# Optimization experiments

Hardware: AMD Instinct MI355X
Metric: run time of the kernel (lower is better)

Reference implementation:

```python
import jax, jax.numpy as jnp
import numpy as np

# VoxelGrid constants (create_empty not shown in source; fixed to a realistic dense grid)
W, L, H = 64, 64, 64
VOXEL_SIZE = 0.05
ORIGIN = 0.0  # per-axis origin, same for all batches
ROUNDING_OFFSET = 0.5
MIN_POINTS_PER_VOXEL = 10


def setup_inputs() -> dict:
    key = jax.random.key(0)
    k1, k2 = jax.random.split(key)
    B, C, N = 4, 32, 200_000
    extent = W * VOXEL_SIZE  # 3.2
    # uniform coords slightly extending past the grid so a few points are OOB
    point_coordinates = jax.random.uniform(
        k1, (B, 3, N), jnp.float32, minval=-0.02, maxval=extent + 0.02)
    point_attributes = jax.random.normal(k2, (B, C, N), jnp.float32)
    return {"point_coordinates": point_coordinates,
            "point_attributes": point_attributes}


def reference(point_coordinates, point_attributes):
    B, C, N = point_attributes.shape
    V = W * L * H
    bounds = jnp.array([W, L, H], jnp.int32)

    # point -> integer voxel coordinates (origin = 0)
    coords = jnp.floor((point_coordinates - ORIGIN) / VOXEL_SIZE
                       + ROUNDING_OFFSET).astype(jnp.int32)      # [B,3,N]
    in_bounds = jnp.all((coords >= 0) & (coords < bounds[None, :, None]),
                        axis=1)                                   # [B,N]
    flat = coords[:, 0] * (L * H) + coords[:, 1] * H + coords[:, 2]
    # route OOB points to segment V which is dropped by segment ops
    flat = jnp.where(in_bounds, flat, V)                          # [B,N]

    def per_batch(idx, attrs, mask):
        # idx [N] int32, attrs [C,N], mask [N] bool
        counts = jax.ops.segment_sum(mask.astype(jnp.int32), idx,
                                     num_segments=V)              # [V]
        vals = jnp.where(mask[None, :], attrs, -jnp.inf)          # [C,N]
        pooled = jax.ops.segment_max(vals.T, idx, num_segments=V).T  # [C,V]
        pooled = jnp.where(counts[None, :] > 0, pooled, jnp.zeros_like(pooled))
        occ = (counts >= MIN_POINTS_PER_VOXEL).astype(attrs.dtype)   # [V]
        return pooled, occ

    data, occ = jax.vmap(per_batch)(flat, point_attributes, in_bounds)
    voxeldata = data.reshape(B, C, W, L, H)
    voxeloccupancy = occ.reshape(B, 1, W, L, H)
    return voxeldata, voxeloccupancy
```

## Files before the change

kernel.cpp:

```cpp
#include <hip/hip_runtime.h>
#include <math.h>


#define GW 64
#define GL 64
#define GH 64
#define GV (GW * GL * GH)
#define NB 4
#define MIN_PTS 10

__device__ __forceinline__ int bin_coord(float x) {
    float m = __fmul_rn(x, 20.0f);
    float r = __fadd_rn(m, 0.5f);
    return (int)floorf(r);
}

__global__ void zero_kernel(uint4* __restrict__ p, int n4) {
    int i = blockIdx.x * blockDim.x + threadIdx.x;
    if (i < n4) p[i] = make_uint4(0u, 0u, 0u, 0u);
}

__global__ void hist_transpose_kernel(const float* __restrict__ coords,
                                      const float* __restrict__ attrs,
                                      int* __restrict__ counts,
                                      int* __restrict__ vox,
                                      int* __restrict__ rank,
                                      float* __restrict__ attrsT,
                                      size_t strideT,
                                      int b0, int N) {
    __shared__ float lds[4][64 * 33];
    int t = threadIdx.x;
    int w = t >> 6;
    int l = t & 63;
    int n = blockIdx.x * 256 + t;
    int b = b0 + blockIdx.y;

    if (n < N) {
        const float* pc = coords + (size_t)b * 3 * N;
        int ix = bin_coord(pc[n]);
        int iy = bin_coord(pc[n + N]);
        int iz = bin_coord(pc[n + 2 * N]);
        bool ok = (unsigned)ix < (unsigned)GW && (unsigned)iy < (unsigned)GL &&
                  (unsigned)iz < (unsigned)GH;
        int v = ok ? ((ix << 12) | (iy << 6) | iz) : -1;
        vox[(size_t)b * N + n] = v;
        if (ok) rank[(size_t)b * N + n] = atomicAdd(&counts[b * GV + v], 1);

        const float* pa = attrs + (size_t)b * 32 * N + n;
        float* row = &lds[w][l * 33];
#pragma unroll
        for (int c = 0; c < 32; ++c)
            row[c] = pa[(size_t)c * N];
    }
    __syncthreads();

    float* dbase = attrsT + (size_t)blockIdx.y * strideT;
    int wbase = blockIdx.x * 256 + w * 64;
    int j = l & 7;
#pragma unroll
    for (int s = 0; s < 8; ++s) {
        int q = s * 8 + (l >> 3);
        int p = wbase + q;
        if (p < N) {
            const float* src = &lds[w][q * 33 + j * 4];
            float4 val = make_float4(src[0], src[1], src[2], src[3]);
            *(float4*)&dbase[(size_t)p * 32 + j * 4] = val;
        }
    }
}

__global__ void hist_kernel(const float* __restrict__ coords,
                            int* __restrict__ counts,
                            int* __restrict__ vox,
                            int* __restrict__ rank,
                            int N) {
    int n = blockIdx.x * blockDim.x + threadIdx.x;
    int b = blockIdx.y;
    if (n >= N) return;
    const float* pc = coords + (size_t)b * 3 * N;
    int ix = bin_coord(pc[n]);
    int iy = bin_coord(pc[n + N]);
    int iz = bin_coord(pc[n + 2 * N]);
    bool ok = (unsigned)ix < (unsigned)GW && (unsigned)iy < (unsigned)GL &&
              (unsigned)iz < (unsigned)GH;
    int v = ok ? ((ix << 12) | (iy << 6) | iz) : -1;
    vox[(size_t)b * N + n] = v;
    if (ok) rank[(size_t)b * N + n] = atomicAdd(&counts[b * GV + v], 1);
}

__global__ void transpose_kernel(const float* __restrict__ attrs,
                                 float* __restrict__ attrsT,
                                 size_t strideT, int b0, int N) {
    __shared__ float lds[4][64 * 33];
    int t = threadIdx.x;
    int w = t >> 6;
    int l = t & 63;
    int n = blockIdx.x * 256 + t;
    int b = b0 + blockIdx.y;
    if (n < N) {
        const float* pa = attrs + (size_t)b * 32 * N + n;
        float* row = &lds[w][l * 33];
#pragma unroll
        for (int c = 0; c < 32; ++c)
            row[c] = pa[(size_t)c * N];
    }
    __syncthreads();
    float* dbase = attrsT + (size_t)blockIdx.y * strideT;
    int wbase = blockIdx.x * 256 + w * 64;
    int j = l & 7;
#pragma unroll
    for (int s = 0; s < 8; ++s) {
        int q = s * 8 + (l >> 3);
        int p = wbase + q;
        if (p < N) {
            const float* src = &lds[w][q * 33 + j * 4];
            float4 val = make_float4(src[0], src[1], src[2], src[3]);
            *(float4*)&dbase[(size_t)p * 32 + j * 4] = val;
        }
    }
}

__global__ void scan_blocks_kernel(const int* __restrict__ counts,
                                   int* __restrict__ offsets,
                                   int* __restrict__ blocksums) {
    __shared__ int lds[256];
    int t = threadIdx.x;
    int base = blockIdx.x * 1024 + t * 4;
    int4 c = *(const int4*)&counts[base];
    int s0 = c.x, s1 = s0 + c.y, s2 = s1 + c.z, s3 = s2 + c.w;
    lds[t] = s3;
    __syncthreads();
    for (int d = 1; d < 256; d <<= 1) {
        int v = (t >= d) ? lds[t - d] : 0;
        __syncthreads();
        if (t >= d) lds[t] += v;
        __syncthreads();
    }
    int excl = (t > 0) ? lds[t - 1] : 0;
    int4 o;
    o.x = excl; o.y = excl + s0; o.z = excl + s1; o.w = excl + s2;
    *(int4*)&offsets[base] = o;
    if (t == 255) blocksums[blockIdx.x] = lds[255];
}

__global__ void scan_sums_kernel(int* __restrict__ blocksums) {
    __shared__ int lds[256];
    int t = threadIdx.x;
    int4 c = *(const int4*)&blocksums[t * 4];
    int s0 = c.x, s1 = s0 + c.y, s2 = s1 + c.z, s3 = s2 + c.w;
    lds[t] = s3;
    __syncthreads();
    for (int d = 1; d < 256; d <<= 1) {
        int v = (t >= d) ? lds[t - d] : 0;
        __syncthreads();
        if (t >= d) lds[t] += v;
        __syncthreads();
    }
    int excl = (t > 0) ? lds[t - 1] : 0;
    int4 o;
    o.x = excl; o.y = excl + s0; o.z = excl + s1; o.w = excl + s2;
    *(int4*)&blocksums[t * 4] = o;
}

__global__ void scan_add_kernel(int* __restrict__ offsets,
                                const int* __restrict__ blocksums) {
    int i = blockIdx.x * blockDim.x + threadIdx.x;
    int s = blocksums[(i * 4) >> 10];
    int4 o = *(int4*)&offsets[i * 4];
    o.x += s; o.y += s; o.z += s; o.w += s;
    *(int4*)&offsets[i * 4] = o;
}

__global__ void scatter_idx_kernel(const int* __restrict__ vox,
                                   const int* __restrict__ rank,
                                   const int* __restrict__ offsets,
                                   int* __restrict__ sorted_idx,
                                   int N) {
    int n = blockIdx.x * blockDim.x + threadIdx.x;
    int b = blockIdx.y;
    if (n >= N) return;
    int v = vox[(size_t)b * N + n];
    if (v < 0) return;
    sorted_idx[offsets[b * GV + v] + rank[(size_t)b * N + n]] = n;
}

__global__ void segmax4_kernel(const float* __restrict__ attrsT,
                               const int* __restrict__ counts,
                               const int* __restrict__ offsets,
                               const int* __restrict__ sorted_idx,
                               float* __restrict__ vdata,
                               float* __restrict__ occ,
                               size_t strideT,
                               int b0) {
    __shared__ float acc[64 * 33];
    __shared__ int cnt_l[64];
    __shared__ int off_l[64];
    __shared__ int sidx[512];
    int t = threadIdx.x;
    int w = t >> 6;
    int l = t & 63;
    int vo = l >> 3;
    int j = l & 7;
    int b = b0 + blockIdx.y;
    int v0 = blockIdx.x * 64;

    if (t < 64) {
        int bv = b * GV + v0 + t;
        cnt_l[t] = counts[bv];
        off_l[t] = offsets[bv];
    }
    __syncthreads();
    int off0 = off_l[0];
    int npts = off_l[63] + cnt_l[63] - off0;

    int vl0 = w * 16 + vo;
    int vl1 = w * 16 + 8 + vo;
    int ks0 = off_l[vl0] - off0, ke0 = ks0 + cnt_l[vl0];
    int ks1 = off_l[vl1] - off0, ke1 = ks1 + cnt_l[vl1];

    float4 m0 = make_float4(-INFINITY, -INFINITY, -INFINITY, -INFINITY);
    float4 m1 = m0;
    const float* sbase = attrsT + (size_t)blockIdx.y * strideT;
    const int* sgl = sorted_idx + off0;

    for (int base = 0; base < npts; base += 512) {
        __syncthreads();
        int mm = npts - base; if (mm > 512) mm = 512;
        for (int i = t; i < mm; i += 256) sidx[i] = sgl[base + i];
        __syncthreads();
        int hi = base + mm;
        int lo0 = ks0 > base ? ks0 : base, h0 = ke0 < hi ? ke0 : hi;
        for (int k = lo0; k < h0; ++k) {
            int idx = sidx[k - base];
            float4 x = *(const float4*)&sbase[(size_t)idx * 32 + j * 4];
            m0.x = fmaxf(m0.x, x.x); m0.y = fmaxf(m0.y, x.y);
            m0.z = fmaxf(m0.z, x.z); m0.w = fmaxf(m0.w, x.w);
        }
        int lo1 = ks1 > base ? ks1 : base, h1 = ke1 < hi ? ke1 : hi;
        for (int k = lo1; k < h1; ++k) {
            int idx = sidx[k - base];
            float4 x = *(const float4*)&sbase[(size_t)idx * 32 + j * 4];
            m1.x = fmaxf(m1.x, x.x); m1.y = fmaxf(m1.y, x.y);
            m1.z = fmaxf(m1.z, x.z); m1.w = fmaxf(m1.w, x.w);
        }
    }

    int c4 = j * 4;
    bool nz0 = cnt_l[vl0] > 0, nz1 = cnt_l[vl1] > 0;
    acc[vl0 * 33 + c4 + 0] = nz0 ? m0.x : 0.0f;
    acc[vl0 * 33 + c4 + 1] = nz0 ? m0.y : 0.0f;
    acc[vl0 * 33 + c4 + 2] = nz0 ? m0.z : 0.0f;
    acc[vl0 * 33 + c4 + 3] = nz0 ? m0.w : 0.0f;
    acc[vl1 * 33 + c4 + 0] = nz1 ? m1.x : 0.0f;
    acc[vl1 * 33 + c4 + 1] = nz1 ? m1.y : 0.0f;
    acc[vl1 * 33 + c4 + 2] = nz1 ? m1.z : 0.0f;
    acc[vl1 * 33 + c4 + 3] = nz1 ? m1.w : 0.0f;
    __syncthreads();

    int vv = v0 + l;
#pragma unroll
    for (int cc = 0; cc < 8; ++cc) {
        int ch = cc * 4 + w;
        vdata[(((size_t)(b * 32 + ch)) << 18) + vv] = acc[l * 33 + ch];
    }
    if (t < 64)
        occ[b * GV + v0 + t] = (cnt_l[t] >= MIN_PTS) ? 1.0f : 0.0f;
}

__global__ void segmax_kernel(const float* __restrict__ attrs,
                              const int* __restrict__ counts,
                              const int* __restrict__ offsets,
                              const int* __restrict__ sorted_idx,
                              float* __restrict__ vdata,
                              float* __restrict__ occ,
                              int N) {
    int t = blockIdx.x * blockDim.x + threadIdx.x;
    int v = t & (GV - 1);
    int c = (t >> 18) & 31;
    int b = t >> 23;
    int bv = (b << 18) | v;
    int cnt = counts[bv];
    int off = offsets[bv];
    const float* row = attrs + ((size_t)(b * 32 + c)) * N;
    float m = -INFINITY;
    for (int k = 0; k < cnt; ++k) {
        m = fmaxf(m, row[sorted_idx[off + k]]);
    }
    vdata[((size_t)(b * 32 + c) << 18) | v] = (cnt > 0) ? m : 0.0f;
    if (c == 0) occ[bv] = (cnt >= MIN_PTS) ? 1.0f : 0.0f;
}

__device__ __forceinline__ unsigned enc_f32(float f) {
    unsigned u = __float_as_uint(f);
    return (u & 0x80000000u) ? ~u : (u | 0x80000000u);
}
__device__ __forceinline__ float dec_f32(unsigned u) {
    return (u & 0x80000000u) ? __uint_as_float(u & 0x7FFFFFFFu)
                             : __uint_as_float(~u);
}

__global__ void init_kernel(uint4* __restrict__ data4, uint4* __restrict__ cnt4,
                            int nData4, int nCnt4) {
    int i = blockIdx.x * blockDim.x + threadIdx.x;
    uint4 z = make_uint4(0u, 0u, 0u, 0u);
    if (i < nData4) data4[i] = z;
    else if (i < nData4 + nCnt4) cnt4[i - nData4] = z;
}

__global__ void scatter_kernel(const float* __restrict__ coords,
                               const float* __restrict__ attrs,
                               unsigned* __restrict__ bits,
                               int* __restrict__ counts,
                               int N, int C) {
    int n = blockIdx.x * blockDim.x + threadIdx.x;
    int b = blockIdx.y;
    if (n >= N) return;
    const float* pc = coords + (size_t)b * 3 * N;
    int ix = bin_coord(pc[n]);
    int iy = bin_coord(pc[n + N]);
    int iz = bin_coord(pc[n + 2 * N]);
    if ((unsigned)ix >= (unsigned)GW || (unsigned)iy >= (unsigned)GL ||
        (unsigned)iz >= (unsigned)GH)
        return;
    int v = (ix << 12) | (iy << 6) | iz;
    atomicAdd(&counts[b * GV + v], 1);
    const float* pa = attrs + (size_t)b * C * N + n;
    unsigned* pb = bits + (size_t)b * C * GV + v;
    for (int c = 0; c < C; ++c)
        atomicMax(&pb[(size_t)c * GV], enc_f32(pa[(size_t)c * N]));
}

__global__ void finalize_kernel(unsigned* __restrict__ data,
                                const int* __restrict__ counts,
                                float* __restrict__ occ, int C) {
    int i = blockIdx.x * blockDim.x + threadIdx.x;
    int nData4 = NB * C * GV / 4;
    int nOcc4 = NB * GV / 4;
    if (i < nData4) {
        int idx = i << 2;
        int v = idx & (GV - 1);
        int b = idx / (C * GV);
        int4 cv = *(const int4*)&counts[b * GV + v];
        uint4 u = *(const uint4*)&data[idx];
        float4 r;
        r.x = cv.x > 0 ? dec_f32(u.x) : 0.0f;
        r.y = cv.y > 0 ? dec_f32(u.y) : 0.0f;
        r.z = cv.z > 0 ? dec_f32(u.z) : 0.0f;
        r.w = cv.w > 0 ? dec_f32(u.w) : 0.0f;
        *(float4*)&data[idx] = r;
    } else if (i < nData4 + nOcc4) {
        int j = (i - nData4) << 2;
        int4 cv = *(const int4*)&counts[j];
        float4 r;
        r.x = cv.x >= MIN_PTS ? 1.0f : 0.0f;
        r.y = cv.y >= MIN_PTS ? 1.0f : 0.0f;
        r.z = cv.z >= MIN_PTS ? 1.0f : 0.0f;
        r.w = cv.w >= MIN_PTS ? 1.0f : 0.0f;
        *(float4*)&occ[j] = r;
    }
}

extern "C" void kernel_launch(void* const* d_in, const int* in_sizes, int n_in,
                              void* d_out, int out_size, void* d_ws, size_t ws_size,
                              hipStream_t stream) {
    const float* coords = (const float*)d_in[0];
    const float* attrs  = (const float*)d_in[1];
    int N = in_sizes[0] / (NB * 3);
    int C = in_sizes[1] / (NB * N);

    size_t wsCommon = (size_t)(2 * NB * GV + 4096 + 3 * NB * N) * 4;
    size_t oneT  = (size_t)N * 32 * 4;
    size_t fullT = (size_t)NB * N * 32 * 4;

    if (C == 32 && ws_size >= wsCommon + oneT) {
        int* counts     = (int*)d_ws;
        int* offsets    = counts + (size_t)NB * GV;
        int* blocksums  = offsets + (size_t)NB * GV;
        int* vox        = blocksums + 4096;
        int* rank       = vox + (size_t)NB * N;
        int* sorted_idx = rank + (size_t)NB * N;
        float* attrsT   = (float*)(sorted_idx + (size_t)NB * N);
        float* vdata    = (float*)d_out;
        float* occ      = (float*)d_out + (size_t)NB * 32 * GV;

        int nCnt4 = NB * GV / 4;
        zero_kernel<<<(nCnt4 + 255) / 256, 256, 0, stream>>>((uint4*)counts,
                                                             nCnt4);
        dim3 pgrid((N + 255) / 256, NB);
        bool full = (ws_size >= wsCommon + fullT);

        if (full) {
            hist_transpose_kernel<<<pgrid, 256, 0, stream>>>(
                coords, attrs, counts, vox, rank, attrsT, (size_t)N * 32, 0, N);
        } else {
            hist_kernel<<<pgrid, 256, 0, stream>>>(coords, counts, vox, rank,
                                                   N);
        }

        scan_blocks_kernel<<<NB * GV / 1024, 256, 0, stream>>>(counts, offsets,
                                                               blocksums);
        scan_sums_kernel<<<1, 256, 0, stream>>>(blocksums);
        scan_add_kernel<<<NB * GV / 1024, 256, 0, stream>>>(offsets, blocksums);

        scatter_idx_kernel<<<pgrid, 256, 0, stream>>>(vox, rank, offsets,
                                                      sorted_idx, N);

        if (full) {
            segmax4_kernel<<<dim3(GV / 64, NB), 256, 0, stream>>>(
                attrsT, counts, offsets, sorted_idx, vdata, occ,
                (size_t)N * 32, 0);
        } else {
            for (int b = 0; b < NB; ++b) {
                transpose_kernel<<<dim3((N + 255) / 256, 1), 256, 0, stream>>>(
                    attrs, attrsT, 0, b, N);
                segmax4_kernel<<<dim3(GV / 64, 1), 256, 0, stream>>>(
                    attrsT, counts, offsets, sorted_idx, vdata, occ, 0, b);
            }
        }
    } else if (C == 32 &&
               ws_size >= (size_t)(2 * NB * GV + 4096 + 3 * NB * N) * 4) {
        int* counts     = (int*)d_ws;
        int* offsets    = counts + (size_t)NB * GV;
        int* blocksums  = offsets + (size_t)NB * GV;
        int* vox        = blocksums + 4096;
        int* rank       = vox + (size_t)NB * N;
        int* sorted_idx = rank + (size_t)NB * N;
        float* vdata    = (float*)d_out;
        float* occ      = (float*)d_out + (size_t)NB * 32 * GV;

        int nCnt4 = NB * GV / 4;
        zero_kernel<<<(nCnt4 + 255) / 256, 256, 0, stream>>>((uint4*)counts,
                                                             nCnt4);
        dim3 pgrid((N + 255) / 256, NB);
        hist_kernel<<<pgrid, 256, 0, stream>>>(coords, counts, vox, rank, N);

        scan_blocks_kernel<<<NB * GV / 1024, 256, 0, stream>>>(counts, offsets,
                                                               blocksums);
        scan_sums_kernel<<<1, 256, 0, stream>>>(blocksums);
        scan_add_kernel<<<NB * GV / 1024, 256, 0, stream>>>(offsets, blocksums);

        scatter_idx_kernel<<<pgrid, 256, 0, stream>>>(vox, rank, offsets,
                                                      sorted_idx, N);

        int segThreads = NB * 32 * GV;
        segmax_kernel<<<segThreads / 256, 256, 0, stream>>>(
            attrs, counts, offsets, sorted_idx, vdata, occ, N);
    } else {
        unsigned* bits = (unsigned*)d_out;
        float* occ = (float*)d_out + (size_t)NB * C * GV;
        int* counts = (int*)d_ws;
        int nData4 = NB * C * GV / 4;
        int nCnt4 = NB * GV / 4;
        int initTotal = nData4 + nCnt4;
        init_kernel<<<(initTotal + 255) / 256, 256, 0, stream>>>(
            (uint4*)d_out, (uint4*)d_ws, nData4, nCnt4);
        dim3 sgrid((N + 255) / 256, NB);
        scatter_kernel<<<sgrid, 256, 0, stream>>>(coords, attrs, bits, counts,
                                                  N, C);
        finalize_kernel<<<(initTotal + 255) / 256, 256, 0, stream>>>(
            bits, counts, occ, C);
    }
}
```

Measured before the change: 300.5 us.

## Fuse the whole voxel pooling pipeline into one cooperative persistent kernel

Replaces the sequence of zero, histogram/transpose, three-stage scan, index scatter and segment-max launches with a single cooperative kernel. The phases are separated by grid-wide syncs and the blocks loop persistently over the work. This is meant to remove per-launch overhead and inter-kernel gaps. In exchange, the grid is capped at occupancy (max 2048 blocks), which can reduce latency hiding in the memory-bound gather phase, and each grid.sync has its own cost. A fallback to the old multi-kernel path remains if the cooperative launch fails.

```diff
diff --git a/kernel.cpp b/kernel.cpp
--- a/kernel.cpp
+++ b/kernel.cpp
@@ -1,4 +1,5 @@
 #include <hip/hip_runtime.h>
+#include <hip/hip_cooperative_groups.h>
 #include <math.h>
 
 
@@ -9,11 +10,214 @@
 #define NB 4
 #define MIN_PTS 10
 
+namespace cg = cooperative_groups;
+
 __device__ __forceinline__ int bin_coord(float x) {
     float m = __fmul_rn(x, 20.0f);
     float r = __fadd_rn(m, 0.5f);
     return (int)floorf(r);
 }
+
+union MegaSmem {
+    float tr[4][64 * 33];
+    int scan[256];
+    struct {
+        float acc[64 * 33];
+        int cnt[64];
+        int off[64];
+        int sidx[512];
+    } sm;
+};
+
+__global__ void __launch_bounds__(256, 4)
+mega_kernel(const float* __restrict__ coords,
+            const float* __restrict__ attrs,
+            int* __restrict__ counts,
+            int* __restrict__ offsets,
+            int* __restrict__ blocksums,
+            int* __restrict__ vox,
+            int* __restrict__ rank,
+            int* __restrict__ sorted_idx,
+            float* __restrict__ attrsT,
+            float* __restrict__ vdata,
+            float* __restrict__ occ,
+            int N) {
+    cg::grid_group grid = cg::this_grid();
+    __shared__ MegaSmem S;
+    const int t = threadIdx.x;
+    const int G = gridDim.x;
+    const int bid = blockIdx.x;
+    const size_t strideT = (size_t)N * 32;
+
+    {
+        uint4* c4 = (uint4*)counts;
+        for (int i = bid * 256 + t; i < NB * GV / 4; i += G * 256)
+            c4[i] = make_uint4(0u, 0u, 0u, 0u);
+    }
+    grid.sync();
+
+    const int perB = (N + 255) / 256;
+    const int w = t >> 6, l = t & 63;
+    for (int vb = bid; vb < NB * perB; vb += G) {
+        int b = vb / perB;
+        int blk = vb - b * perB;
+        int n = blk * 256 + t;
+        if (n < N) {
+            const float* pc = coords + (size_t)b * 3 * N;
+            int ix = bin_coord(pc[n]);
+            int iy = bin_coord(pc[n + N]);
+            int iz = bin_coord(pc[n + 2 * N]);
+            bool ok = (unsigned)ix < (unsigned)GW &&
+                      (unsigned)iy < (unsigned)GL &&
+                      (unsigned)iz < (unsigned)GH;
+            int v = ok ? ((ix << 12) | (iy << 6) | iz) : -1;
+            vox[(size_t)b * N + n] = v;
+            if (ok) rank[(size_t)b * N + n] = atomicAdd(&counts[b * GV + v], 1);
+            const float* pa = attrs + (size_t)b * 32 * N + n;
+            float* row = &S.tr[w][l * 33];
+#pragma unroll
+            for (int c = 0; c < 32; ++c)
+                row[c] = pa[(size_t)c * N];
+        }
+        __syncthreads();
+        float* dbase = attrsT + (size_t)b * strideT;
+        int wbase = blk * 256 + w * 64;
+        int j = l & 7;
+#pragma unroll
+        for (int s = 0; s < 8; ++s) {
+            int q = s * 8 + (l >> 3);
+            int p = wbase + q;
+            if (p < N) {
+                const float* src = &S.tr[w][q * 33 + j * 4];
+                float4 val = make_float4(src[0], src[1], src[2], src[3]);
+                *(float4*)&dbase[(size_t)p * 32 + j * 4] = val;
+            }
+        }
+        __syncthreads();
+    }
+    grid.sync();
+
+    for (int sb = bid; sb < NB * GV / 1024; sb += G) {
+        int base = sb * 1024 + t * 4;
+        int4 c = *(const int4*)&counts[base];
+        int s0 = c.x, s1 = s0 + c.y, s2 = s1 + c.z, s3 = s2 + c.w;
+        S.scan[t] = s3;
+        __syncthreads();
+        for (int d = 1; d < 256; d <<= 1) {
+            int v = (t >= d) ? S.scan[t - d] : 0;
+            __syncthreads();
+            if (t >= d) S.scan[t] += v;
+            __syncthreads();
+        }
+        int excl = (t > 0) ? S.scan[t - 1] : 0;
+        int4 o;
+        o.x = excl; o.y = excl + s0; o.z = excl + s1; o.w = excl + s2;
+        *(int4*)&offsets[base] = o;
+        if (t == 255) blocksums[sb] = S.scan[255];
+        __syncthreads();
+    }
+    grid.sync();
+
+    if (bid == 0) {
+        int4 c = *(const int4*)&blocksums[t * 4];
+        int s0 = c.x, s1 = s0 + c.y, s2 = s1 + c.z, s3 = s2 + c.w;
+        S.scan[t] = s3;
+        __syncthreads();
+        for (int d = 1; d < 256; d <<= 1) {
+            int v = (t >= d) ? S.scan[t - d] : 0;
+            __syncthreads();
+            if (t >= d) S.scan[t] += v;
+            __syncthreads();
+        }
+        int excl = (t > 0) ? S.scan[t - 1] : 0;
+        int4 o;
+        o.x = excl; o.y = excl + s0; o.z = excl + s1; o.w = excl + s2;
+        *(int4*)&blocksums[t * 4] = o;
+    }
+    grid.sync();
+
+    for (int i = bid * 256 + t; i < NB * GV / 4; i += G * 256) {
+        int s = blocksums[(i * 4) >> 10];
+        int4 o = *(int4*)&offsets[i * 4];
+        o.x += s; o.y += s; o.z += s; o.w += s;
+        *(int4*)&offsets[i * 4] = o;
+    }
+    grid.sync();
+
+    for (int i = bid * 256 + t; i < NB * N; i += G * 256) {
+        int b = i / N;
+        int n = i - b * N;
+        int v = vox[i];
+        if (v >= 0)
+            sorted_idx[offsets[b * GV + v] + rank[i]] = n;
+    }
+    grid.sync();
+
+    const int vo = l >> 3;
+    const int j = l & 7;
+    for (int vb = bid; vb < NB * (GV / 64); vb += G) {
+        int b = vb >> 12;
+        int v0 = (vb & 4095) * 64;
+        __syncthreads();
+        if (t < 64) {
+            int bv = b * GV + v0 + t;
+            S.sm.cnt[t] = counts[bv];
+            S.sm.off[t] = offsets[bv];
+        }
+        __syncthreads();
+        int off0 = S.sm.off[0];
+        int npts = S.sm.off[63] + S.sm.cnt[63] - off0;
+        int vl0 = w * 16 + vo;
+        int vl1 = w * 16 + 8 + vo;
+        int ks0 = S.sm.off[vl0] - off0, ke0 = ks0 + S.sm.cnt[vl0];
+        int ks1 = S.sm.off[vl1] - off0, ke1 = ks1 + S.sm.cnt[vl1];
+        float4 m0 = make_float4(-INFINITY, -INFINITY, -INFINITY, -INFINITY);
+        float4 m1 = m0;
+        const float* sbase = attrsT + (size_t)b * strideT;
+        const int* sgl = sorted_idx + off0;
+        for (int base = 0; base < npts; base += 512) {
+            __syncthreads();
+            int mm = npts - base; if (mm > 512) mm = 512;
+            for (int i = t; i < mm; i += 256) S.sm.sidx[i] = sgl[base + i];
+            __syncthreads();
+            int hi = base + mm;
+            int lo0 = ks0 > base ? ks0 : base, h0 = ke0 < hi ? ke0 : hi;
+            for (int k = lo0; k < h0; ++k) {
+                int idx = S.sm.sidx[k - base];
+                float4 x = *(const float4*)&sbase[(size_t)idx * 32 + j * 4];
+                m0.x = fmaxf(m0.x, x.x); m0.y = fmaxf(m0.y, x.y);
+                m0.z = fmaxf(m0.z, x.z); m0.w = fmaxf(m0.w, x.w);
+            }
+            int lo1 = ks1 > base ? ks1 : base, h1 = ke1 < hi ? ke1 : hi;
+            for (int k = lo1; k < h1; ++k) {
+                int idx = S.sm.sidx[k - base];
+                float4 x = *(const float4*)&sbase[(size_t)idx * 32 + j * 4];
+                m1.x = fmaxf(m1.x, x.x); m1.y = fmaxf(m1.y, x.y);
+                m1.z = fmaxf(m1.z, x.z); m1.w = fmaxf(m1.w, x.w);
+            }
+        }
+        int c4 = j * 4;
+        bool nz0 = S.sm.cnt[vl0] > 0, nz1 = S.sm.cnt[vl1] > 0;
+        S.sm.acc[vl0 * 33 + c4 + 0] = nz0 ? m0.x : 0.0f;
+        S.sm.acc[vl0 * 33 + c4 + 1] = nz0 ? m0.y : 0.0f;
+        S.sm.acc[vl0 * 33 + c4 + 2] = nz0 ? m0.z : 0.0f;
+        S.sm.acc[vl0 * 33 + c4 + 3] = nz0 ? m0.w : 0.0f;
+        S.sm.acc[vl1 * 33 + c4 + 0] = nz1 ? m1.x : 0.0f;
+        S.sm.acc[vl1 * 33 + c4 + 1] = nz1 ? m1.y : 0.0f;
+        S.sm.acc[vl1 * 33 + c4 + 2] = nz1 ? m1.z : 0.0f;
+        S.sm.acc[vl1 * 33 + c4 + 3] = nz1 ? m1.w : 0.0f;
+        __syncthreads();
+        int vv = v0 + l;
+#pragma unroll
+        for (int cc = 0; cc < 8; ++cc) {
+            int ch = cc * 4 + w;
+            vdata[(((size_t)(b * 32 + ch)) << 18) + vv] = S.sm.acc[l * 33 + ch];
+        }
+        if (t < 64)
+            occ[b * GV + v0 + t] = (S.sm.cnt[t] >= MIN_PTS) ? 1.0f : 0.0f;
+    }
+}
+
 
 __global__ void zero_kernel(uint4* __restrict__ p, int n4) {
     int i = blockIdx.x * blockDim.x + threadIdx.x;
@@ -26,15 +230,13 @@
                                       int* __restrict__ vox,
                                       int* __restrict__ rank,
                                       float* __restrict__ attrsT,
-                                      size_t strideT,
-                                      int b0, int N) {
+                                      size_t strideT, int b0, int N) {
     __shared__ float lds[4][64 * 33];
     int t = threadIdx.x;
     int w = t >> 6;
     int l = t & 63;
     int n = blockIdx.x * 256 + t;
     int b = b0 + blockIdx.y;
-
     if (n < N) {
         const float* pc = coords + (size_t)b * 3 * N;
         int ix = bin_coord(pc[n]);
@@ -45,7 +247,6 @@
         int v = ok ? ((ix << 12) | (iy << 6) | iz) : -1;
         vox[(size_t)b * N + n] = v;
         if (ok) rank[(size_t)b * N + n] = atomicAdd(&counts[b * GV + v], 1);
-
         const float* pa = attrs + (size_t)b * 32 * N + n;
         float* row = &lds[w][l * 33];
 #pragma unroll
@@ -53,7 +254,6 @@
             row[c] = pa[(size_t)c * N];
     }
     __syncthreads();
-
     float* dbase = attrsT + (size_t)blockIdx.y * strideT;
     int wbase = blockIdx.x * 256 + w * 64;
     int j = l & 7;
@@ -190,8 +390,7 @@
                                const int* __restrict__ sorted_idx,
                                float* __restrict__ vdata,
                                float* __restrict__ occ,
-                               size_t strideT,
-                               int b0) {
+                               size_t strideT, int b0) {
     __shared__ float acc[64 * 33];
     __shared__ int cnt_l[64];
     __shared__ int off_l[64];
@@ -203,7 +402,6 @@
     int j = l & 7;
     int b = b0 + blockIdx.y;
     int v0 = blockIdx.x * 64;
-
     if (t < 64) {
         int bv = b * GV + v0 + t;
         cnt_l[t] = counts[bv];
@@ -212,17 +410,14 @@
     __syncthreads();
     int off0 = off_l[0];
     int npts = off_l[63] + cnt_l[63] - off0;
-
     int vl0 = w * 16 + vo;
     int vl1 = w * 16 + 8 + vo;
     int ks0 = off_l[vl0] - off0, ke0 = ks0 + cnt_l[vl0];
     int ks1 = off_l[vl1] - off0, ke1 = ks1 + cnt_l[vl1];
-
     float4 m0 = make_float4(-INFINITY, -INFINITY, -INFINITY, -INFINITY);
     float4 m1 = m0;
     const float* sbase = attrsT + (size_t)blockIdx.y * strideT;
     const int* sgl = sorted_idx + off0;
-
     for (int base = 0; base < npts; base += 512) {
         __syncthreads();
         int mm = npts - base; if (mm > 512) mm = 512;
@@ -244,7 +439,6 @@
             m1.z = fmaxf(m1.z, x.z); m1.w = fmaxf(m1.w, x.w);
         }
     }
-
     int c4 = j * 4;
     bool nz0 = cnt_l[vl0] > 0, nz1 = cnt_l[vl1] > 0;
     acc[vl0 * 33 + c4 + 0] = nz0 ? m0.x : 0.0f;
@@ -256,7 +450,6 @@
     acc[vl1 * 33 + c4 + 2] = nz1 ? m1.z : 0.0f;
     acc[vl1 * 33 + c4 + 3] = nz1 ? m1.w : 0.0f;
     __syncthreads();
-
     int vv = v0 + l;
 #pragma unroll
     for (int cc = 0; cc < 8; ++cc) {
@@ -381,44 +574,82 @@
         int* sorted_idx = rank + (size_t)NB * N;
         float* attrsT   = (float*)(sorted_idx + (size_t)NB * N);
         float* vdata    = (float*)d_out;
-        float* occ      = (float*)d_out + (size_t)NB * 32 * GV;
-
-        int nCnt4 = NB * GV / 4;
-        zero_kernel<<<(nCnt4 + 255) / 256, 256, 0, stream>>>((uint4*)counts,
-                                                             nCnt4);
-        dim3 pgrid((N + 255) / 256, NB);
+        float* occp     = (float*)d_out + (size_t)NB * 32 * GV;
+
         bool full = (ws_size >= wsCommon + fullT);
+        bool launched = false;
 
         if (full) {
-            hist_transpose_kernel<<<pgrid, 256, 0, stream>>>(
-                coords, attrs, counts, vox, rank, attrsT, (size_t)N * 32, 0, N);
-        } else {
-            hist_kernel<<<pgrid, 256, 0, stream>>>(coords, counts, vox, rank,
-                                                   N);
-        }
-
-        scan_blocks_kernel<<<NB * GV / 1024, 256, 0, stream>>>(counts, offsets,
-                                                               blocksums);
-        scan_sums_kernel<<<1, 256, 0, stream>>>(blocksums);
-        scan_add_kernel<<<NB * GV / 1024, 256, 0, stream>>>(offsets, blocksums);
-
-        scatter_idx_kernel<<<pgrid, 256, 0, stream>>>(vox, rank, offsets,
-                                                      sorted_idx, N);
-
-        if (full) {
-            segmax4_kernel<<<dim3(GV / 64, NB), 256, 0, stream>>>(
-                attrsT, counts, offsets, sorted_idx, vdata, occ,
-                (size_t)N * 32, 0);
-        } else {
-            for (int b = 0; b < NB; ++b) {
-                transpose_kernel<<<dim3((N + 255) / 256, 1), 256, 0, stream>>>(
-                    attrs, attrsT, 0, b, N);
-                segmax4_kernel<<<dim3(GV / 64, 1), 256, 0, stream>>>(
-                    attrsT, counts, offsets, sorted_idx, vdata, occ, 0, b);
+            static int coopGrid = -2;
+            if (coopGrid == -2) {
+                int maxB = 0;
+                if (hipOccupancyMaxActiveBlocksPerMultiprocessor(
+                        &maxB, mega_kernel, 256, 0) == hipSuccess && maxB > 0) {
+                    int cus = 256;
+                    int dev = 0;
+                    static hipDeviceProp_t prop;
+                    if (hipGetDevice(&dev) == hipSuccess &&
+                        hipGetDeviceProperties(&prop, dev) == hipSuccess &&
+                        prop.multiProcessorCount > 0)
+                        cus = prop.multiProcessorCount;
+                    coopGrid = maxB * cus;
+                    if (coopGrid > 2048) coopGrid = 2048;
+                } else {
+                    coopGrid = 0;
+                }
             }
-        }
-    } else if (C == 32 &&
-               ws_size >= (size_t)(2 * NB * GV + 4096 + 3 * NB * N) * 4) {
+            if (coopGrid > 0) {
+                void* kargs[] = {
+                    (void*)&coords, (void*)&attrs, (void*)&counts,
+                    (void*)&offsets, (void*)&blocksums, (void*)&vox,
+                    (void*)&rank, (void*)&sorted_idx, (void*)&attrsT,
+                    (void*)&vdata, (void*)&occp, (void*)&N};
+                hipError_t e = hipLaunchCooperativeKernel(
+                    reinterpret_cast<const void*>(mega_kernel),
+                    dim3((unsigned)coopGrid), dim3(256), kargs, 0, stream);
+                if (e == hipSuccess) {
+                    launched = true;
+                } else {
+                    (void)hipGetLastError();
+                    coopGrid = 0;
+                }
+            }
+        }
+
+        if (!launched) {
+            int nCnt4 = NB * GV / 4;
+            zero_kernel<<<(nCnt4 + 255) / 256, 256, 0, stream>>>(
+                (uint4*)counts, nCnt4);
+            dim3 pgrid((N + 255) / 256, NB);
+            if (full) {
+                hist_transpose_kernel<<<pgrid, 256, 0, stream>>>(
+                    coords, attrs, counts, vox, rank, attrsT,
+                    (size_t)N * 32, 0, N);
+            } else {
+                hist_kernel<<<pgrid, 256, 0, stream>>>(coords, counts, vox,
+                                                       rank, N);
+            }
+            scan_blocks_kernel<<<NB * GV / 1024, 256, 0, stream>>>(
+                counts, offsets, blocksums);
+            scan_sums_kernel<<<1, 256, 0, stream>>>(blocksums);
+            scan_add_kernel<<<NB * GV / 1024, 256, 0, stream>>>(offsets,
+                                                                blocksums);
+            scatter_idx_kernel<<<pgrid, 256, 0, stream>>>(vox, rank, offsets,
+                                                          sorted_idx, N);
+            if (full) {
+                segmax4_kernel<<<dim3(GV / 64, NB), 256, 0, stream>>>(
+                    attrsT, counts, offsets, sorted_idx, vdata, occp,
+                    (size_t)N * 32, 0);
+            } else {
+                for (int b = 0; b < NB; ++b) {
+                    transpose_kernel<<<dim3((N + 255) / 256, 1), 256, 0,
+                                       stream>>>(attrs, attrsT, 0, b, N);
+                    segmax4_kernel<<<dim3(GV / 64, 1), 256, 0, stream>>>(
+                        attrsT, counts, offsets, sorted_idx, vdata, occp, 0, b);
+                }
+            }
+        }
+    } else if (C == 32 && ws_size >= wsCommon) {
         int* counts     = (int*)d_ws;
         int* offsets    = counts + (size_t)NB * GV;
         int* blocksums  = offsets + (size_t)NB * GV;
@@ -426,28 +657,25 @@
         int* rank       = vox + (size_t)NB * N;
         int* sorted_idx = rank + (size_t)NB * N;
         float* vdata    = (float*)d_out;
-        float* occ      = (float*)d_out + (size_t)NB * 32 * GV;
+        float* occp     = (float*)d_out + (size_t)NB * 32 * GV;
 
         int nCnt4 = NB * GV / 4;
         zero_kernel<<<(nCnt4 + 255) / 256, 256, 0, stream>>>((uint4*)counts,
                                                              nCnt4);
         dim3 pgrid((N + 255) / 256, NB);
         hist_kernel<<<pgrid, 256, 0, stream>>>(coords, counts, vox, rank, N);
-
         scan_blocks_kernel<<<NB * GV / 1024, 256, 0, stream>>>(counts, offsets,
                                                                blocksums);
         scan_sums_kernel<<<1, 256, 0, stream>>>(blocksums);
         scan_add_kernel<<<NB * GV / 1024, 256, 0, stream>>>(offsets, blocksums);
-
         scatter_idx_kernel<<<pgrid, 256, 0, stream>>>(vox, rank, offsets,
                                                       sorted_idx, N);
-
         int segThreads = NB * 32 * GV;
         segmax_kernel<<<segThreads / 256, 256, 0, stream>>>(
-            attrs, counts, offsets, sorted_idx, vdata, occ, N);
+            attrs, counts, offsets, sorted_idx, vdata, occp, N);
     } else {
         unsigned* bits = (unsigned*)d_out;
-        float* occ = (float*)d_out + (size_t)NB * C * GV;
+        float* occp = (float*)d_out + (size_t)NB * C * GV;
         int* counts = (int*)d_ws;
         int nData4 = NB * C * GV / 4;
         int nCnt4 = NB * GV / 4;
@@ -458,6 +686,6 @@
         scatter_kernel<<<sgrid, 256, 0, stream>>>(coords, attrs, bits, counts,
                                                   N, C);
         finalize_kernel<<<(initTotal + 255) / 256, 256, 0, stream>>>(
-            bits, counts, occ, C);
-    }
-}
+            bits, counts, occp, C);
+    }
+}
```

After: 959.9 us. 3.19x slower.
